# Optimization experiments

Measured on AMD Instinct MI355X. Metric: run time of the kernel, lower is better.

The kernel has to match this reference:

```python
import jax, jax.numpy as jnp
import numpy as np

N_NODES = 10000
N_EDGES = 160000
MUL = 128            # multiplicity of 0e and 1o node feature irreps
N_RADIAL = 8
AVG_NEIGH = 16.0
INV_SQRT3 = float(1.0 / np.sqrt(3.0))  # w3j(1,1,0) contraction factor (component norm)


def setup_inputs() -> dict:
    key = jax.random.key(0)
    ks = jax.random.split(key, 16)
    node_feats = jax.random.normal(ks[0], (N_NODES, MUL + 3 * MUL), jnp.float32)
    edge_attrs = jax.random.normal(ks[1], (N_EDGES, 4), jnp.float32)      # sph harms l=0,1
    edge_feats = jax.random.normal(ks[2], (N_EDGES, N_RADIAL), jnp.float32)
    lengths = jax.random.uniform(ks[3], (N_EDGES, 1), jnp.float32)
    edge_index = jax.random.randint(ks[4], (2, N_EDGES), 0, N_NODES)
    d_in = 2 * MUL + N_RADIAL + 1  # 265: sender scalars + receiver scalars + radial + length
    def lin(k, sh):
        return jax.random.normal(k, sh, jnp.float32) / np.sqrt(sh[0])
    # last MLP layer: variance_scaling(scale=1e-6, fan_avg, uniform)
    fan_avg = (MUL + 4 * MUL) / 2.0
    lim = float(np.sqrt(3.0 * (0.001 ** 2) / fan_avg))
    return dict(
        node_feats=node_feats, edge_attrs=edge_attrs, edge_feats=edge_feats,
        lengths=lengths, edge_index=edge_index,
        W_scalar=lin(ks[5], (MUL, MUL)),
        W_up0=lin(ks[6], (MUL, MUL)),
        W_up1=lin(ks[7], (MUL, MUL)),
        W_mlp1=lin(ks[8], (d_in, MUL)), b_mlp1=jnp.zeros((MUL,), jnp.float32),
        W_mlp2=lin(ks[9], (MUL, MUL)), b_mlp2=jnp.zeros((MUL,), jnp.float32),
        W_mlp3=jax.random.uniform(ks[10], (MUL, 4 * MUL), jnp.float32, -lim, lim),
        W_out0=lin(ks[11], (2 * MUL, MUL)),
        W_out1=lin(ks[12], (2 * MUL, MUL)),
    )


def reference(node_feats, edge_attrs, edge_feats, lengths, edge_index,
              W_scalar, W_up0, W_up1, W_mlp1, b_mlp1, W_mlp2, b_mlp2, W_mlp3,
              W_out0, W_out1):
    sender, receiver = edge_index[0], edge_index[1]
    s_in = node_feats[:, :MUL]                        # [N, 128] 0e
    v_in = node_feats[:, MUL:].reshape(-1, MUL, 3)    # [N, 128, 3] 1o
    inv = 1.0 / np.sqrt(MUL)
    # linear_scalar / linear_up (e3nn Linear, element path normalization)
    node_scalars = (s_in @ W_scalar) * inv            # [N, 128]
    s_up = (s_in @ W_up0) * inv                       # [N, 128]
    v_up = jnp.einsum('nui,uw->nwi', v_in, W_up1) * inv  # [N, 128, 3]
    # per-edge MLP -> tensor-product weights (Dense-SiLU-Dense-SiLU-Dense)
    mlp_in = jnp.concatenate([node_scalars[sender], node_scalars[receiver],
                              edge_feats, lengths], axis=-1)  # [E, 265]
    h = jax.nn.silu(mlp_in @ W_mlp1 + b_mlp1)
    h = jax.nn.silu(h @ W_mlp2 + b_mlp2)
    tpw = h @ W_mlp3                                  # [E, 512]
    w0, w1, w2, w3 = jnp.split(tpw, 4, axis=-1)       # one [E,128] block per TP path
    # gather sender features; split edge sph harms
    se = s_up[sender]                                 # [E, 128]
    ve = v_up[sender]                                 # [E, 128, 3]
    y0 = edge_attrs[:, 0:1]                           # [E, 1]
    y1 = edge_attrs[:, 1:4]                           # [E, 3]
    # equivariant 'uvu' tensor product (component irrep normalization)
    m0a = w0 * se * y0                                                # 0e x 0e -> 0e
    m0b = w3 * jnp.einsum('eui,ei->eu', ve, y1) * INV_SQRT3           # 1o x 1o -> 0e
    m1a = (w1 * se)[:, :, None] * y1[:, None, :]                      # 0e x 1o -> 1o
    m1b = (w2 * y0)[:, :, None] * ve                                  # 1o x 0e -> 1o
    mji = jnp.concatenate([m0a, m0b,
                           m1a.reshape(N_EDGES, -1),
                           m1b.reshape(N_EDGES, -1)], axis=-1)        # [E, 1024]
    # scatter-sum aggregate over receivers
    msg = jax.ops.segment_sum(mji, receiver, num_segments=N_NODES)    # [N, 1024]
    ms = msg[:, :2 * MUL]                             # [N, 256]  (two 0e blocks)
    mv = msg[:, 2 * MUL:].reshape(-1, 2 * MUL, 3)     # [N, 256, 3] (two 1o blocks)
    # final e3nn Linear (irreps_mid -> target) then / avg_num_neighbors
    inv2 = 1.0 / np.sqrt(2 * MUL)
    out_s = (ms @ W_out0) * (inv2 / AVG_NEIGH)                        # [N, 128]
    out_v = jnp.einsum('nui,uw->nwi', mv, W_out1) * (inv2 / AVG_NEIGH)  # [N, 128, 3]
    # reshape_irreps: [N, mul, (lmax+1)^2] = [N, 128, 4]
    return jnp.concatenate([out_s[:, :, None], out_v], axis=-1)
```

## Files before the change

### kernel.cpp

```cpp
#include <hip/hip_runtime.h>

#define N_NODESC 10000
#define N_EDGESC 160000
#define NBLK_TOT 2500
#define NP       (N_NODESC*128)
#define INV128   0.08838834764831845f
#define INV_SQRT3C 0.5773502691896258f
#define SCALE_OUT 0.00390625f

typedef __attribute__((ext_vector_type(8))) short bf16x8;
typedef __attribute__((ext_vector_type(4))) float f32x4;

__device__ __forceinline__ float silu_f(float x) {
  return x / (1.f + __expf(-x));
}
__device__ __forceinline__ ushort f2bf_rne(float x) {
  uint u = __float_as_uint(x);
  uint r = (u + 0x7FFFu + ((u >> 16) & 1u)) >> 16;
  return (ushort)r;
}
__device__ __forceinline__ float bf2f(ushort h) {
  return __uint_as_float(((uint)h) << 16);
}

__global__ __launch_bounds__(256) void k_histprep(
    const int* __restrict__ eidx, int* __restrict__ deg,
    const float* __restrict__ W2, const float* __restrict__ W3,
    const float* __restrict__ Wu0, const float* __restrict__ Wu1,
    const float* __restrict__ Wo0, const float* __restrict__ Wo1,
    ushort* __restrict__ TT) {
  const int bid = blockIdx.x;
  if (bid < 625) {
    int e = bid * 256 + threadIdx.x;
    if (e < N_EDGESC) atomicAdd(&deg[eidx[N_EDGESC + e]], 1);
    return;
  }
  int id = (bid - 625) * 256 + threadIdx.x;
  if (id < 16384) {
    int k = id >> 7, n = id & 127;
    float v = W2[k * 128 + n];
    ushort hi = f2bf_rne(v);
    TT[4 * 16384 + n * 128 + k] = hi;
    TT[5 * 16384 + n * 128 + k] = f2bf_rne(v - bf2f(hi));
  } else if (id < 81920) {
    int s = id - 16384;
    int k = s >> 9, col = s & 511;
    int cb = col >> 7, n = col & 127;
    TT[(6 + cb) * 16384 + n * 128 + k] = f2bf_rne(W3[k * 512 + col]);
  } else if (id < 114688) {
    int t = id - 81920;
    int w = t >> 14, r = t & 16383;
    int k = r >> 7, n = r & 127;
    const float* W = w ? Wu1 : Wu0;
    float v = W[k * 128 + n];
    ushort hi = f2bf_rne(v);
    TT[(10 + w * 2) * 16384 + n * 128 + k] = hi;
    TT[(11 + w * 2) * 16384 + n * 128 + k] = f2bf_rne(v - bf2f(hi));
  } else if (id < 180224) {
    int t = id - 114688;
    int w = t >> 15, r = t & 32767;
    int k = r >> 7, n = r & 127;
    const float* W = w ? Wo1 : Wo0;
    float v = W[k * 128 + n];
    int kh = k >> 7, kk = k & 127;
    ushort hi = f2bf_rne(v);
    TT[(16 + w * 4 + kh * 2) * 16384 + n * 128 + kk] = hi;
    TT[(17 + w * 4 + kh * 2) * 16384 + n * 128 + kk] = f2bf_rne(v - bf2f(hi));
  }
}

__global__ __launch_bounds__(1024) void k_scan(const int* __restrict__ deg,
                                               int* __restrict__ row_start,
                                               int* __restrict__ cursor) {
  __shared__ int buf[1024];
  const int t = threadIdx.x;
  for (int i = t; i < N_NODESC; i += 1024) cursor[i] = 0;
  int d[10];
  int loc = 0;
  #pragma unroll
  for (int i = 0; i < 10; i++) {
    int n = t * 10 + i;
    d[i] = (n < N_NODESC) ? deg[n] : 0;
    loc += d[i];
  }
  buf[t] = loc;
  __syncthreads();
  int v = loc;
  for (int off = 1; off < 1024; off <<= 1) {
    int u = (t >= off) ? buf[t - off] : 0;
    __syncthreads();
    v += u;
    buf[t] = v;
    __syncthreads();
  }
  int run = v - loc;
  #pragma unroll
  for (int i = 0; i < 10; i++) {
    int n = t * 10 + i;
    if (n < N_NODESC) row_start[n] = run;
    run += d[i];
  }
  if (t == 1023) row_start[N_NODESC] = v;
}

__global__ __launch_bounds__(256) void k_scatter(const int* __restrict__ eidx,
                                                 const int* __restrict__ row_start,
                                                 int* __restrict__ cursor,
                                                 int* __restrict__ perm) {
  int e = blockIdx.x * 256 + threadIdx.x;
  if (e < N_EDGESC) {
    int r = eidx[N_EDGESC + e];
    int pos = row_start[r] + atomicAdd(&cursor[r], 1);
    perm[pos] = e;
  }
}

__global__ __launch_bounds__(256) void k_wcomp(
    const float* __restrict__ Wsc, const float* __restrict__ W1,
    ushort* __restrict__ TT) {
  __shared__ float sA2[64][132];
  __shared__ float sW2[128][128];
  const int rh = blockIdx.x;
  const int wb = blockIdx.y;
  for (int idx = threadIdx.x; idx < 128 * 32; idx += 256) {
    int k = idx >> 5, fc = (idx & 31) << 2;
    *(float4*)&sW2[k][fc] = *(const float4*)&W1[(wb * 128 + k) * 128 + fc];
  }
  for (int idx = threadIdx.x; idx < 64 * 32; idx += 256) {
    int i = idx >> 5, fc = (idx & 31) << 2;
    *(float4*)&sA2[i][fc] = *(const float4*)&Wsc[(rh * 64 + i) * 128 + fc];
  }
  __syncthreads();
  const int r0 = (threadIdx.x >> 4) * 4;
  const int c0 = (threadIdx.x & 15) * 8;
  float acc[4][8] = {};
  #pragma unroll 4
  for (int k = 0; k < 128; k++) {
    float a[4];
    #pragma unroll
    for (int j = 0; j < 4; j++) a[j] = sA2[r0 + j][k];
    float w[8];
    *(float4*)&w[0] = *(const float4*)&sW2[k][c0];
    *(float4*)&w[4] = *(const float4*)&sW2[k][c0 + 4];
    #pragma unroll
    for (int j = 0; j < 4; j++)
      #pragma unroll
      for (int c = 0; c < 8; c++) acc[j][c] += a[j] * w[c];
  }
  #pragma unroll
  for (int j = 0; j < 4; j++) {
    int u = rh * 64 + r0 + j;
    #pragma unroll
    for (int c = 0; c < 8; c++) {
      float v = acc[j][c];
      ushort hi = f2bf_rne(v);
      TT[(wb * 2 + 0) * 16384 + (c0 + c) * 128 + u] = hi;
      TT[(wb * 2 + 1) * 16384 + (c0 + c) * 128 + u] = f2bf_rne(v - bf2f(hi));
    }
  }
}

#define GEMM_PASS1(ACC)                                                        \
  _Pragma("unroll") for (int s = 0; s < 4; s++) {                              \
    bf16x8 ah = *(const bf16x8*)&sAh[ar][s * 32 + lq * 8];                     \
    _Pragma("unroll") for (int nt = 0; nt < 8; nt++) {                         \
      bf16x8 bb = *(const bf16x8*)&sB[nt * 16 + ln][s * 32 + lq * 8];          \
      ACC[nt] = __builtin_amdgcn_mfma_f32_16x16x32_bf16(ah, bb, ACC[nt], 0, 0, 0); \
    }                                                                          \
  }

#define STAGEB(T) { uint4 tv[8];                                               \
  _Pragma("unroll") for (int i = 0; i < 8; i++)                                \
    tv[i] = ttp[(T) * 2048 + cid + 256 * i];                                   \
  _Pragma("unroll") for (int i = 0; i < 8; i++) {                              \
    int c = cid + 256 * i;                                                     \
    *(uint4*)&sB[c >> 4][(c & 15) * 8] = tv[i]; } }

__global__ __launch_bounds__(256, 3) void k_node_up(
    const float* __restrict__ nf,
    const ushort* __restrict__ TT,
    float* __restrict__ P1s,
    float* __restrict__ P1r,
    float* __restrict__ SU,
    float* __restrict__ VU,
    int* __restrict__ perm,
    const int* __restrict__ row_start)
{
  __shared__ ushort sAh[64][132];
  __shared__ ushort sB[128][132];
  const int n0 = blockIdx.x * 64;
  const int which = blockIdx.y;
  const int cid = threadIdx.x;
  const int wid = cid >> 6;
  const int lane = cid & 63;
  const int lq = lane >> 4;
  const int ln = lane & 15;
  const int ar = wid * 16 + ln;
  const uint4* ttp = (const uint4*)TT;

  if (which == 4) {
    int n = blockIdx.x * 256 + cid;
    if (n < N_NODESC) {
      int s = row_start[n], e = row_start[n + 1];
      for (int i = s + 1; i < e; i++) {
        int key = perm[i];
        int j = i - 1;
        while (j >= s && perm[j] > key) { perm[j + 1] = perm[j]; j--; }
        perm[j + 1] = key;
      }
    }
    return;
  }

  if (which == 0) {
    for (int idx = cid; idx < 64 * 32; idx += 256) {
      int r = idx >> 5, fc = (idx & 31) << 2;
      int n = n0 + r;
      float4 v = {0.f, 0.f, 0.f, 0.f};
      if (n < N_NODESC) v = *(const float4*)&nf[(size_t)n * 512 + fc];
      float vv[4] = {v.x, v.y, v.z, v.w};
      #pragma unroll
      for (int j = 0; j < 4; j++) sAh[r][fc + j] = f2bf_rne(vv[j]);
    }
    for (int g = 0; g < 3; g++) {
      if (g) __syncthreads();
      const int tA = (g == 2) ? 10 : g * 2;
      STAGEB(tA)
      __syncthreads();
      f32x4 acc[8];
      #pragma unroll
      for (int nt = 0; nt < 8; nt++) acc[nt] = (f32x4){0.f, 0.f, 0.f, 0.f};
      GEMM_PASS1(acc)
      __syncthreads();
      STAGEB(tA + 1)
      __syncthreads();
      GEMM_PASS1(acc)
      float* op = (g == 0) ? P1s : ((g == 1) ? P1r : SU);
      #pragma unroll
      for (int q = 0; q < 4; q++) {
        int n = n0 + wid * 16 + lq * 4 + q;
        if (n < N_NODESC) {
          #pragma unroll
          for (int nt = 0; nt < 8; nt++)
            op[(size_t)n * 128 + nt * 16 + ln] = acc[nt][q] * INV128;
        }
      }
    }
  } else {
    int comp = which - 1;
    for (int idx = cid; idx < 64 * 128; idx += 256) {
      int r = idx >> 7, u = idx & 127;
      int n = n0 + r;
      float v = (n < N_NODESC) ? nf[(size_t)n * 512 + 128 + u * 3 + comp] : 0.f;
      sAh[r][u] = f2bf_rne(v);
    }
    STAGEB(12)
    __syncthreads();
    f32x4 acc[8];
    #pragma unroll
    for (int nt = 0; nt < 8; nt++) acc[nt] = (f32x4){0.f, 0.f, 0.f, 0.f};
    GEMM_PASS1(acc)
    __syncthreads();
    STAGEB(13)
    __syncthreads();
    GEMM_PASS1(acc)
    float* op = VU + (size_t)comp * NP;
    #pragma unroll
    for (int q = 0; q < 4; q++) {
      int n = n0 + wid * 16 + lq * 4 + q;
      if (n < N_NODESC) {
        #pragma unroll
        for (int nt = 0; nt < 8; nt++)
          op[(size_t)n * 128 + nt * 16 + ln] = acc[nt][q] * INV128;
      }
    }
  }
}

#define REDUCE(P, MI) {                                                        \
  const int ntask = sNseg << 7;                                                \
  for (int task = cid; task < ntask; task += 256) {                            \
    const int si = task >> 7, col = task & 127;                                \
    const int s = sSegStart[si], e = sSegStart[si + 1];                        \
    float sum = 0.f;                                                           \
    int e2 = s;                                                                \
    for (; e2 + 8 <= e; e2 += 8) {                                             \
      float m0 = sMsg[e2][col],     m1 = sMsg[e2 + 1][col];                    \
      float m2 = sMsg[e2 + 2][col], m3 = sMsg[e2 + 3][col];                    \
      float m4 = sMsg[e2 + 4][col], m5 = sMsg[e2 + 5][col];                    \
      float m6 = sMsg[e2 + 6][col], m7 = sMsg[e2 + 7][col];                    \
      if ((MI) >= 0) {                                                         \
        const int mi = (MI) >= 0 ? (MI) : 0;                                   \
        sum += m0 * sY4[e2][mi];     sum += m1 * sY4[e2 + 1][mi];              \
        sum += m2 * sY4[e2 + 2][mi]; sum += m3 * sY4[e2 + 3][mi];              \
        sum += m4 * sY4[e2 + 4][mi]; sum += m5 * sY4[e2 + 5][mi];              \
        sum += m6 * sY4[e2 + 6][mi]; sum += m7 * sY4[e2 + 7][mi];              \
      } else { sum += m0; sum += m1; sum += m2; sum += m3;                     \
               sum += m4; sum += m5; sum += m6; sum += m7; }                   \
    }                                                                          \
    for (; e2 < e; e2++) {                                                     \
      float mv = sMsg[e2][col];                                                \
      sum += ((MI) >= 0) ? mv * sY4[e2][(MI) >= 0 ? (MI) : 0] : mv;            \
    }                                                                          \
    if (si == 0 && contF)                                                      \
      CONT[(size_t)gblk * 1024 + (P) * 128 + col] = sum;                       \
    else                                                                       \
      MSG[(size_t)(P) * NP + (size_t)sSegNode[si] * 128 + col] = sum;          \
  } }

#define REDUCE3 {                                                              \
  const int ntask = sNseg << 7;                                                \
  for (int task = cid; task < ntask; task += 256) {                            \
    const int si = task >> 7, col = task & 127;                                \
    const int s = sSegStart[si], e = sSegStart[si + 1];                        \
    float s0 = 0.f, s1 = 0.f, s2 = 0.f;                                        \
    int e2 = s;                                                                \
    for (; e2 + 4 <= e; e2 += 4) {                                             \
      _Pragma("unroll") for (int u = 0; u < 4; u++) {                          \
        float mv = sMsg[e2 + u][col];                                          \
        s0 += mv * sY4[e2 + u][1];                                             \
        s1 += mv * sY4[e2 + u][2];                                             \
        s2 += mv * sY4[e2 + u][3];                                             \
      }                                                                        \
    }                                                                          \
    for (; e2 < e; e2++) {                                                     \
      float mv = sMsg[e2][col];                                                \
      s0 += mv * sY4[e2][1]; s1 += mv * sY4[e2][2]; s2 += mv * sY4[e2][3];     \
    }                                                                          \
    if (si == 0 && contF) {                                                    \
      CONT[(size_t)gblk * 1024 + 2 * 128 + col] = s0;                          \
      CONT[(size_t)gblk * 1024 + 3 * 128 + col] = s1;                          \
      CONT[(size_t)gblk * 1024 + 4 * 128 + col] = s2;                          \
    } else {                                                                   \
      size_t nb = (size_t)sSegNode[si] * 128 + col;                            \
      MSG[2 * (size_t)NP + nb] = s0;                                           \
      MSG[3 * (size_t)NP + nb] = s1;                                           \
      MSG[4 * (size_t)NP + nb] = s2;                                           \
    }                                                                          \
  } }

__global__ __launch_bounds__(256, 3) void k_edge_fused(
    const float* __restrict__ P1s,
    const float* __restrict__ P1r,
    const float* __restrict__ SU,
    const float* __restrict__ VU,
    const float* __restrict__ ef,
    const float* __restrict__ len,
    const float* __restrict__ ea,
    const int* __restrict__ eidx,
    const int* __restrict__ perm,
    const int* __restrict__ row_start,
    const float* __restrict__ W1,
    const float* __restrict__ b1,
    const float* __restrict__ b2,
    const ushort* __restrict__ TT,
    float* __restrict__ MSG,
    float* __restrict__ CONT)
{
  __shared__ ushort sAh[64][132];
  __shared__ ushort sB[128][132];
  __shared__ float sY4[64][4];
  __shared__ int sSnd[64], sRcv[64], sEid[64];
  __shared__ int sSegStart[65], sSegNode[64];
  __shared__ int sNseg, sContFirst;
  float (*sMsg)[132] = (float (*)[132])&sB[0][0];

  const int bid = blockIdx.x;
  const int xcd = bid & 7, sub = bid >> 3;
  const int gblk = (xcd < 4) ? (xcd * 313 + sub)
                             : (1252 + (xcd - 4) * 312 + sub);
  const int j0 = gblk * 64;
  const int cid = threadIdx.x;
  const int wid = cid >> 6;
  const int lane = cid & 63;
  const int lq = lane >> 4;
  const int ln = lane & 15;
  const int ar = wid * 16 + ln;
  const uint4* ttp = (const uint4*)TT;

  if (cid < 64) {
    int r = cid;
    int e = perm[j0 + r];
    int snd = eidx[e];
    int rcv = eidx[N_EDGESC + e];
    sSnd[r] = snd;
    sRcv[r] = rcv;
    sEid[r] = e;
    *(float4*)&sY4[r][0] = *(const float4*)&ea[(size_t)e * 4];
    int prev = __shfl_up(rcv, 1);
    bool flag = (r == 0) || (rcv != prev);
    unsigned long long mask = __ballot(flag ? 1 : 0);
    if (flag) {
      int rank = __popcll(mask & ((1ull << r) - 1ull));
      sSegStart[rank] = r;
      sSegNode[rank] = rcv;
    }
    if (r == 0) {
      sNseg = __popcll(mask);
      sContFirst = (row_start[rcv] != j0) ? 1 : 0;
    }
    if (r == 63) sSegStart[__popcll(mask)] = 64;
  }
  __syncthreads();
  const bool contF = (sContFirst != 0);

  for (int idx = cid; idx < 64 * 32; idx += 256) {
    int r = idx >> 5, c4 = (idx & 31) << 2;
    int ns = sSnd[r], nr = sRcv[r];
    float4 a = *(const float4*)&P1s[(size_t)ns * 128 + c4];
    float4 b = *(const float4*)&P1r[(size_t)nr * 128 + c4];
    int e = sEid[r];
    float el[9];
    float4 e0 = *(const float4*)&ef[(size_t)e * 8];
    float4 e1 = *(const float4*)&ef[(size_t)e * 8 + 4];
    el[0] = e0.x; el[1] = e0.y; el[2] = e0.z; el[3] = e0.w;
    el[4] = e1.x; el[5] = e1.y; el[6] = e1.z; el[7] = e1.w;
    el[8] = len[e];
    float4 bb = *(const float4*)&b1[c4];
    float v[4] = {a.x + b.x + bb.x, a.y + b.y + bb.y,
                  a.z + b.z + bb.z, a.w + b.w + bb.w};
    #pragma unroll
    for (int t = 0; t < 9; t++) {
      float4 wt = *(const float4*)&W1[(size_t)(256 + t) * 128 + c4];
      float elt = el[t];
      v[0] += elt * wt.x; v[1] += elt * wt.y;
      v[2] += elt * wt.z; v[3] += elt * wt.w;
    }
    #pragma unroll
    for (int j = 0; j < 4; j++)
      sAh[r][c4 + j] = f2bf_rne(silu_f(v[j]));
  }
  STAGEB(4)
  __syncthreads();

  f32x4 acc2[8];
  #pragma unroll
  for (int nt = 0; nt < 8; nt++) acc2[nt] = (f32x4){0.f, 0.f, 0.f, 0.f};
  GEMM_PASS1(acc2)
  __syncthreads();
  STAGEB(5)
  __syncthreads();
  GEMM_PASS1(acc2)
  __syncthreads();
  #pragma unroll
  for (int nt = 0; nt < 8; nt++) {
    int col = nt * 16 + ln;
    float bb2 = b2[col];
    #pragma unroll
    for (int q = 0; q < 4; q++) {
      int rr = wid * 16 + lq * 4 + q;
      sAh[rr][col] = f2bf_rne(silu_f(acc2[nt][q] + bb2));
    }
  }

  int erow[4], esnd[4];
  float y0r[4], y1r3[4][3];
  #pragma unroll
  for (int q = 0; q < 4; q++) {
    int rr = wid * 16 + lq * 4 + q;
    erow[q] = rr;
    esnd[q] = sSnd[rr];
    y0r[q] = sY4[rr][0];
    #pragma unroll
    for (int i = 0; i < 3; i++) y1r3[q][i] = sY4[rr][1 + i];
  }
  float se[4][8];
  #pragma unroll
  for (int q = 0; q < 4; q++)
    #pragma unroll
    for (int nt = 0; nt < 8; nt++)
      se[q][nt] = SU[(size_t)esnd[q] * 128 + nt * 16 + ln];
  float dacc[4][8];

  STAGEB(6)
  __syncthreads();

  {
    f32x4 acc3[8];
    #pragma unroll
    for (int nt = 0; nt < 8; nt++) acc3[nt] = (f32x4){0.f, 0.f, 0.f, 0.f};
    GEMM_PASS1(acc3)
    __syncthreads();
    #pragma unroll
    for (int q = 0; q < 4; q++)
      #pragma unroll
      for (int nt = 0; nt < 8; nt++)
        sMsg[erow[q]][nt * 16 + ln] = acc3[nt][q] * se[q][nt] * y0r[q];
    __syncthreads();
    REDUCE(0, -1)
    __syncthreads();
    STAGEB(7)
    __syncthreads();
  }
  {
    f32x4 acc3[8];
    #pragma unroll
    for (int nt = 0; nt < 8; nt++) acc3[nt] = (f32x4){0.f, 0.f, 0.f, 0.f};
    GEMM_PASS1(acc3)
    __syncthreads();
    #pragma unroll
    for (int q = 0; q < 4; q++)
      #pragma unroll
      for (int nt = 0; nt < 8; nt++)
        sMsg[erow[q]][nt * 16 + ln] = acc3[nt][q] * se[q][nt];
    __syncthreads();
    REDUCE3
    __syncthreads();
    STAGEB(8)
    __syncthreads();
  }
  {
    f32x4 acc3[8];
    #pragma unroll
    for (int nt = 0; nt < 8; nt++) acc3[nt] = (f32x4){0.f, 0.f, 0.f, 0.f};
    GEMM_PASS1(acc3)
    __syncthreads();
    for (int pi = 0; pi < 3; pi++) {
      float vu[4][8];
      #pragma unroll
      for (int q = 0; q < 4; q++)
        #pragma unroll
        for (int nt = 0; nt < 8; nt++) {
          vu[q][nt] = VU[(size_t)pi * NP + (size_t)esnd[q] * 128 + nt * 16 + ln];
          if (pi == 0) dacc[q][nt] = vu[q][nt] * y1r3[q][0];
          else dacc[q][nt] += vu[q][nt] * y1r3[q][pi];
        }
      #pragma unroll
      for (int q = 0; q < 4; q++)
        #pragma unroll
        for (int nt = 0; nt < 8; nt++)
          sMsg[erow[q]][nt * 16 + ln] = acc3[nt][q] * vu[q][nt];
      __syncthreads();
      if (pi == 0) { REDUCE(5, 0) }
      else if (pi == 1) { REDUCE(6, 0) }
      else { REDUCE(7, 0) }
      __syncthreads();
    }
    STAGEB(9)
    __syncthreads();
  }
  {
    f32x4 acc3[8];
    #pragma unroll
    for (int nt = 0; nt < 8; nt++) acc3[nt] = (f32x4){0.f, 0.f, 0.f, 0.f};
    GEMM_PASS1(acc3)
    __syncthreads();
    #pragma unroll
    for (int q = 0; q < 4; q++)
      #pragma unroll
      for (int nt = 0; nt < 8; nt++)
        sMsg[erow[q]][nt * 16 + ln] = acc3[nt][q] * dacc[q][nt] * INV_SQRT3C;
    __syncthreads();
    REDUCE(1, -1)
  }
}

__global__ __launch_bounds__(256) void k_fixup(float* __restrict__ MSG,
                                               const float* __restrict__ CONT,
                                               const int* __restrict__ row_start) {
  int t = blockIdx.x * 256 + threadIdx.x;
  int n = t >> 5;
  int c4 = (t & 31) * 4;
  if (n >= N_NODESC) return;
  int s = row_start[n], e = row_start[n + 1];
  if (e <= s) {
    float4 z = {0.f, 0.f, 0.f, 0.f};
    #pragma unroll
    for (int p = 0; p < 8; p++)
      *(float4*)&MSG[(size_t)p * NP + (size_t)n * 128 + c4] = z;
    return;
  }
  int b0 = s >> 6, b1 = (e - 1) >> 6;
  if (b1 <= b0) return;
  for (int p = 0; p < 8; p++) {
    float4 v = *(float4*)&MSG[(size_t)p * NP + (size_t)n * 128 + c4];
    for (int b = b0 + 1; b <= b1; b++) {
      const float4 u = *(const float4*)&CONT[(size_t)b * 1024 + p * 128 + c4];
      v.x += u.x; v.y += u.y; v.z += u.z; v.w += u.w;
    }
    *(float4*)&MSG[(size_t)p * NP + (size_t)n * 128 + c4] = v;
  }
}

__global__ __launch_bounds__(256, 3) void k_out(
    const float* __restrict__ MSG,
    const ushort* __restrict__ TT,
    float* __restrict__ out)
{
  __shared__ ushort sAh[64][132];
  __shared__ ushort sB[128][132];
  const int n0 = blockIdx.x * 64;
  const int y = blockIdx.y;
  const int cid = threadIdx.x;
  const int wid = cid >> 6;
  const int lane = cid & 63;
  const int lq = lane >> 4;
  const int ln = lane & 15;
  const int ar = wid * 16 + ln;
  const uint4* ttp = (const uint4*)TT;
  const int pA = (y == 0) ? 0 : (1 + y);
  const int pB = (y == 0) ? 1 : (4 + y);
  const int tbase = 16 + ((y == 0) ? 0 : 4);

  f32x4 acc[8];
  #pragma unroll
  for (int nt = 0; nt < 8; nt++) acc[nt] = (f32x4){0.f, 0.f, 0.f, 0.f};

  for (int kh = 0; kh < 2; kh++) {
    if (kh) __syncthreads();
    const int p = kh ? pB : pA;
    for (int idx = cid; idx < 64 * 32; idx += 256) {
      int r = idx >> 5, fc = (idx & 31) << 2;
      int n = n0 + r;
      float4 v = {0.f, 0.f, 0.f, 0.f};
      if (n < N_NODESC) v = *(const float4*)&MSG[(size_t)p * NP + (size_t)n * 128 + fc];
      float vv[4] = {v.x, v.y, v.z, v.w};
      #pragma unroll
      for (int j = 0; j < 4; j++) sAh[r][fc + j] = f2bf_rne(vv[j]);
    }
    STAGEB(tbase + kh * 2)
    __syncthreads();
    GEMM_PASS1(acc)
    __syncthreads();
    STAGEB(tbase + kh * 2 + 1)
    __syncthreads();
    GEMM_PASS1(acc)
  }
  #pragma unroll
  for (int q = 0; q < 4; q++) {
    int n = n0 + wid * 16 + lq * 4 + q;
    if (n < N_NODESC) {
      #pragma unroll
      for (int nt = 0; nt < 8; nt++)
        out[(size_t)n * 512 + (size_t)(nt * 16 + ln) * 4 + y] = acc[nt][q] * SCALE_OUT;
    }
  }
}

extern "C" void kernel_launch(void* const* d_in, const int* in_sizes, int n_in,
                              void* d_out, int out_size, void* d_ws, size_t ws_size,
                              hipStream_t stream) {
  const float* nf  = (const float*)d_in[0];
  const float* ea  = (const float*)d_in[1];
  const float* ef  = (const float*)d_in[2];
  const float* len = (const float*)d_in[3];
  const int*   ei  = (const int*)d_in[4];
  const float* Wsc = (const float*)d_in[5];
  const float* Wu0 = (const float*)d_in[6];
  const float* Wu1 = (const float*)d_in[7];
  const float* W1  = (const float*)d_in[8];
  const float* b1  = (const float*)d_in[9];
  const float* W2  = (const float*)d_in[10];
  const float* b2  = (const float*)d_in[11];
  const float* W3  = (const float*)d_in[12];
  const float* Wo0 = (const float*)d_in[13];
  const float* Wo1 = (const float*)d_in[14];
  float* out = (float*)d_out;
  float* ws  = (float*)d_ws;

  const size_t NPs = (size_t)NP;
  float* P1s  = ws;
  float* P1r  = ws + NPs;
  float* SU   = ws + 2 * NPs;
  float* VU   = ws + 3 * NPs;
  float* MSG  = ws + 6 * NPs;
  float* CONT = ws + 14 * NPs;
  ushort* TT  = (ushort*)(CONT + (size_t)NBLK_TOT * 1024);
  int* perm      = (int*)(TT + 24 * 16384);
  int* deg       = perm + N_EDGESC;
  int* cursor    = deg + N_NODESC;
  int* row_start = cursor + N_NODESC;

  hipMemsetAsync(deg, 0, N_NODESC * sizeof(int), stream);

  k_histprep<<<1329, 256, 0, stream>>>(ei, deg, W2, W3, Wu0, Wu1, Wo0, Wo1, TT);
  k_scan<<<1, 1024, 0, stream>>>(deg, row_start, cursor);
  k_scatter<<<(N_EDGESC + 255) / 256, 256, 0, stream>>>(ei, row_start, cursor, perm);
  k_wcomp<<<dim3(2, 2), 256, 0, stream>>>(Wsc, W1, TT);

  k_node_up<<<dim3(157, 5), 256, 0, stream>>>(nf, TT, P1s, P1r, SU, VU,
                                              perm, row_start);

  k_edge_fused<<<NBLK_TOT, 256, 0, stream>>>(P1s, P1r, SU, VU, ef, len, ea, ei,
                                             perm, row_start, W1, b1, b2, TT,
                                             MSG, CONT);

  k_fixup<<<(N_NODESC * 32 + 255) / 256, 256, 0, stream>>>(MSG, CONT, row_start);
  k_out<<<dim3(157, 4), 256, 0, stream>>>(MSG, TT, out);
}
```

Before: 285.2 us.

## Replace scalar LDS segment reductions with bf16 MFMA one-hot segment-sum matmuls

The per-block segmented reductions over receiver segments are recast as a matmul between a one-hot segment-membership matrix and the transposed per-edge message tile, run on MFMA bf16 instructions. Messages are now rounded to bf16 and stored transposed in shared memory, and the spherical-harmonic weights are folded into each message before the reduction. The goal is to remove the serial, bank-conflict-prone scalar loops whose cost depends on segment length. In exchange, messages lose precision before summation, and the REDUCE3 path now needs three separate passes.

After: 355.8 us. 24.7% more time.

```diff
diff --git a/kernel.cpp b/kernel.cpp
--- a/kernel.cpp
+++ b/kernel.cpp
@@ -277,67 +277,45 @@
   }
 }
 
-#define REDUCE(P, MI) {                                                        \
-  const int ntask = sNseg << 7;                                                \
-  for (int task = cid; task < ntask; task += 256) {                            \
-    const int si = task >> 7, col = task & 127;                                \
-    const int s = sSegStart[si], e = sSegStart[si + 1];                        \
-    float sum = 0.f;                                                           \
-    int e2 = s;                                                                \
-    for (; e2 + 8 <= e; e2 += 8) {                                             \
-      float m0 = sMsg[e2][col],     m1 = sMsg[e2 + 1][col];                    \
-      float m2 = sMsg[e2 + 2][col], m3 = sMsg[e2 + 3][col];                    \
-      float m4 = sMsg[e2 + 4][col], m5 = sMsg[e2 + 5][col];                    \
-      float m6 = sMsg[e2 + 6][col], m7 = sMsg[e2 + 7][col];                    \
-      if ((MI) >= 0) {                                                         \
-        const int mi = (MI) >= 0 ? (MI) : 0;                                   \
-        sum += m0 * sY4[e2][mi];     sum += m1 * sY4[e2 + 1][mi];              \
-        sum += m2 * sY4[e2 + 2][mi]; sum += m3 * sY4[e2 + 3][mi];              \
-        sum += m4 * sY4[e2 + 4][mi]; sum += m5 * sY4[e2 + 5][mi];              \
-        sum += m6 * sY4[e2 + 6][mi]; sum += m7 * sY4[e2 + 7][mi];              \
-      } else { sum += m0; sum += m1; sum += m2; sum += m3;                     \
-               sum += m4; sum += m5; sum += m6; sum += m7; }                   \
-    }                                                                          \
-    for (; e2 < e; e2++) {                                                     \
-      float mv = sMsg[e2][col];                                                \
-      sum += ((MI) >= 0) ? mv * sY4[e2][(MI) >= 0 ? (MI) : 0] : mv;            \
-    }                                                                          \
-    if (si == 0 && contF)                                                      \
-      CONT[(size_t)gblk * 1024 + (P) * 128 + col] = sum;                       \
-    else                                                                       \
-      MSG[(size_t)(P) * NP + (size_t)sSegNode[si] * 128 + col] = sum;          \
-  } }
-
-#define REDUCE3 {                                                              \
-  const int ntask = sNseg << 7;                                                \
-  for (int task = cid; task < ntask; task += 256) {                            \
-    const int si = task >> 7, col = task & 127;                                \
-    const int s = sSegStart[si], e = sSegStart[si + 1];                        \
-    float s0 = 0.f, s1 = 0.f, s2 = 0.f;                                        \
-    int e2 = s;                                                                \
-    for (; e2 + 4 <= e; e2 += 4) {                                             \
-      _Pragma("unroll") for (int u = 0; u < 4; u++) {                          \
-        float mv = sMsg[e2 + u][col];                                          \
-        s0 += mv * sY4[e2 + u][1];                                             \
-        s1 += mv * sY4[e2 + u][2];                                             \
-        s2 += mv * sY4[e2 + u][3];                                             \
+#define MRED(P) {                                                              \
+  __syncthreads();                                         \
+  const int nseg = sNseg;                                                      \
+  f32x4 racc[4][2];                                                            \
+  _Pragma("unroll") for (int mt = 0; mt < 4; mt++)                             \
+    _Pragma("unroll") for (int t = 0; t < 2; t++)                              \
+      racc[mt][t] = (f32x4){0.f, 0.f, 0.f, 0.f};                               \
+  _Pragma("unroll") for (int mt = 0; mt < 4; mt++) {                           \
+    if (mt * 16 < nseg) {                                                      \
+      _Pragma("unroll") for (int s = 0; s < 2; s++) {                          \
+        bf16x8 af;                                                             \
+        _Pragma("unroll") for (int j = 0; j < 8; j++) {                        \
+          int e = s * 32 + lq * 8 + j;                                         \
+          af[j] = (sSegId[e] == mt * 16 + ln) ? (short)0x3F80 : (short)0;      \
+        }                                                                      \
+        _Pragma("unroll") for (int t = 0; t < 2; t++) {                        \
+          bf16x8 bb = *(const bf16x8*)&sMsgT[(wid * 2 + t) * 16 + ln]          \
+                                            [s * 32 + lq * 8];                 \
+          racc[mt][t] = __builtin_amdgcn_mfma_f32_16x16x32_bf16(               \
+              af, bb, racc[mt][t], 0, 0, 0);                                   \
+        }                                                                      \
       }                                                                        \
     }                                                                          \
-    for (; e2 < e; e2++) {                                                     \
-      float mv = sMsg[e2][col];                                                \
-      s0 += mv * sY4[e2][1]; s1 += mv * sY4[e2][2]; s2 += mv * sY4[e2][3];     \
-    }                                                                          \
-    if (si == 0 && contF) {                                                    \
-      CONT[(size_t)gblk * 1024 + 2 * 128 + col] = s0;                          \
-      CONT[(size_t)gblk * 1024 + 3 * 128 + col] = s1;                          \
-      CONT[(size_t)gblk * 1024 + 4 * 128 + col] = s2;                          \
-    } else {                                                                   \
-      size_t nb = (size_t)sSegNode[si] * 128 + col;                            \
-      MSG[2 * (size_t)NP + nb] = s0;                                           \
-      MSG[3 * (size_t)NP + nb] = s1;                                           \
-      MSG[4 * (size_t)NP + nb] = s2;                                           \
-    }                                                                          \
-  } }
+  }                                                                            \
+  _Pragma("unroll") for (int mt = 0; mt < 4; mt++)                             \
+    _Pragma("unroll") for (int t = 0; t < 2; t++)                              \
+      _Pragma("unroll") for (int q = 0; q < 4; q++) {                          \
+        int seg = mt * 16 + lq * 4 + q;                                        \
+        if (seg < nseg) {                                                      \
+          int col = (wid * 2 + t) * 16 + ln;                                   \
+          float val = racc[mt][t][q];                                          \
+          if (seg == 0 && contF)                                               \
+            CONT[(size_t)gblk * 1024 + (P) * 128 + col] = val;                 \
+          else                                                                 \
+            MSG[(size_t)(P) * NP + (size_t)sSegNode[seg] * 128 + col] = val;   \
+        }                                                                      \
+      }                                                                        \
+  __syncthreads();                           \
+}
 
 __global__ __launch_bounds__(256, 3) void k_edge_fused(
     const float* __restrict__ P1s,
@@ -360,10 +338,10 @@
   __shared__ ushort sAh[64][132];
   __shared__ ushort sB[128][132];
   __shared__ float sY4[64][4];
-  __shared__ int sSnd[64], sRcv[64], sEid[64];
+  __shared__ int sSnd[64], sRcv[64], sEid[64], sSegId[64];
   __shared__ int sSegStart[65], sSegNode[64];
   __shared__ int sNseg, sContFirst;
-  float (*sMsg)[132] = (float (*)[132])&sB[0][0];
+  ushort (*sMsgT)[72] = (ushort (*)[72])&sB[0][0];
 
   const int bid = blockIdx.x;
   const int xcd = bid & 7, sub = bid >> 3;
@@ -390,6 +368,7 @@
     int prev = __shfl_up(rcv, 1);
     bool flag = (r == 0) || (rcv != prev);
     unsigned long long mask = __ballot(flag ? 1 : 0);
+    sSegId[r] = __popcll(mask & (~0ull >> (63 - r))) - 1;
     if (flag) {
       int rank = __popcll(mask & ((1ull << r) - 1ull));
       sSegStart[rank] = r;
@@ -485,10 +464,9 @@
     for (int q = 0; q < 4; q++)
       #pragma unroll
       for (int nt = 0; nt < 8; nt++)
-        sMsg[erow[q]][nt * 16 + ln] = acc3[nt][q] * se[q][nt] * y0r[q];
-    __syncthreads();
-    REDUCE(0, -1)
-    __syncthreads();
+        sMsgT[nt * 16 + ln][erow[q]] =
+            f2bf_rne(acc3[nt][q] * se[q][nt] * y0r[q]);
+    MRED(0)
     STAGEB(7)
     __syncthreads();
   }
@@ -499,13 +477,15 @@
     GEMM_PASS1(acc3)
     __syncthreads();
     #pragma unroll
-    for (int q = 0; q < 4; q++)
-      #pragma unroll
-      for (int nt = 0; nt < 8; nt++)
-        sMsg[erow[q]][nt * 16 + ln] = acc3[nt][q] * se[q][nt];
-    __syncthreads();
-    REDUCE3
-    __syncthreads();
+    for (int i = 0; i < 3; i++) {
+      #pragma unroll
+      for (int q = 0; q < 4; q++)
+        #pragma unroll
+        for (int nt = 0; nt < 8; nt++)
+          sMsgT[nt * 16 + ln][erow[q]] =
+              f2bf_rne(acc3[nt][q] * se[q][nt] * y1r3[q][i]);
+      MRED(2 + i)
+    }
     STAGEB(8)
     __syncthreads();
   }
@@ -515,6 +495,7 @@
     for (int nt = 0; nt < 8; nt++) acc3[nt] = (f32x4){0.f, 0.f, 0.f, 0.f};
     GEMM_PASS1(acc3)
     __syncthreads();
+    #pragma unroll
     for (int pi = 0; pi < 3; pi++) {
       float vu[4][8];
       #pragma unroll
@@ -529,12 +510,9 @@
       for (int q = 0; q < 4; q++)
         #pragma unroll
         for (int nt = 0; nt < 8; nt++)
-          sMsg[erow[q]][nt * 16 + ln] = acc3[nt][q] * vu[q][nt];
-      __syncthreads();
-      if (pi == 0) { REDUCE(5, 0) }
-      else if (pi == 1) { REDUCE(6, 0) }
-      else { REDUCE(7, 0) }
-      __syncthreads();
+          sMsgT[nt * 16 + ln][erow[q]] =
+              f2bf_rne(acc3[nt][q] * vu[q][nt] * y0r[q]);
+      MRED(5 + pi)
     }
     STAGEB(9)
     __syncthreads();
@@ -549,9 +527,9 @@
     for (int q = 0; q < 4; q++)
       #pragma unroll
       for (int nt = 0; nt < 8; nt++)
-        sMsg[erow[q]][nt * 16 + ln] = acc3[nt][q] * dacc[q][nt] * INV_SQRT3C;
-    __syncthreads();
-    REDUCE(1, -1)
+        sMsgT[nt * 16 + ln][erow[q]] =
+            f2bf_rne(acc3[nt][q] * dacc[q][nt] * INV_SQRT3C);
+    MRED(1)
   }
 }
 
```
